# Performance work log

Measured on AMD Instinct MI355X. Metric: run time of the kernel, lower is better.

## Reference

```python
import jax, jax.numpy as jnp
import numpy as np

DIM = 512
NUM_HEADS = 8
POS_DIM = 2
K_CLUSTERS = 256
M_PTS = 256


def setup_inputs() -> dict:
    key = jax.random.key(0)
    ks = jax.random.split(key, 9)
    pos = jax.random.uniform(ks[0], (K_CLUSTERS, M_PTS, POS_DIM), dtype=jnp.float32)
    feat = jax.random.normal(ks[1], (K_CLUSTERS, M_PTS, DIM), dtype=jnp.float32)
    mask = jax.random.randint(ks[2], (K_CLUSTERS, M_PTS, 1), 0, 2, dtype=jnp.int32)
    s = 0.02
    qkv_w = jax.random.normal(ks[3], (DIM, 3 * DIM), dtype=jnp.float32) * s
    qkv_b = jnp.zeros((3 * DIM,), dtype=jnp.float32)
    pos_w = jax.random.normal(ks[4], (POS_DIM, NUM_HEADS), dtype=jnp.float32) * s
    pos_b = jnp.zeros((NUM_HEADS,), dtype=jnp.float32)
    proj_w = jax.random.normal(ks[5], (DIM, DIM), dtype=jnp.float32) * s
    proj_b = jnp.zeros((DIM,), dtype=jnp.float32)
    return {"pos": pos, "feat": feat, "qkv_w": qkv_w, "qkv_b": qkv_b,
            "pos_w": pos_w, "pos_b": pos_b, "proj_w": proj_w, "proj_b": proj_b,
            "mask": mask}


def reference(pos, feat, qkv_w, qkv_b, pos_w, pos_b, proj_w, proj_b, mask):
    k_, m, c = feat.shape
    H = pos_w.shape[1]
    hd = c // H
    scale = hd ** -0.5

    # qkv projection -> (3, k, H, m, hd)
    qkv = (feat @ qkv_w + qkv_b).reshape(k_, m, 3, H, hd).transpose(2, 0, 3, 1, 4)
    q, k, v = qkv[0], qkv[1], qkv[2]

    attn = jnp.einsum('khid,khjd->khij', q * scale, k)  # k,H,m,m

    # normalize each coordinate by its global max over all clusters/points
    pos_n = pos / jnp.max(pos, axis=(0, 1), keepdims=True)
    # rel_pos[k,a,b,d] = pos[k,b,d] - pos[k,a,d]
    rel_pos = pos_n[:, None, :, :] - pos_n[:, :, None, :]  # k,m,m,d
    pos_bias = rel_pos @ pos_w + pos_b                      # k,m,m,H
    attn = attn + pos_bias.transpose(0, 3, 1, 2)            # k,H,m,m

    # mask: k,m,1 -> additive bias over key dim
    maskf = mask[:, :, 0].astype(attn.dtype)                # k,m
    attn = attn + ((1.0 - maskf) * -100.0)[:, None, None, :]

    attn = jax.nn.softmax(attn, axis=-1)
    x = jnp.einsum('khij,khjd->khid', attn, v)              # k,H,m,hd
    x = x.transpose(0, 2, 1, 3).reshape(k_, m, c)
    x = x @ proj_w + proj_b
    return x
```

## Files before the change

kernel.cpp:

```cpp
#include <hip/hip_runtime.h>
#include <stdint.h>

typedef short bf16x8 __attribute__((ext_vector_type(8)));
typedef float f32x4 __attribute__((ext_vector_type(4)));
typedef unsigned short u16x4 __attribute__((ext_vector_type(4)));
typedef unsigned short ushort_t;

__device__ __forceinline__ float bf2f(unsigned short u) {
    union { unsigned int i; float f; } v; v.i = ((unsigned int)u) << 16; return v.f;
}
__device__ __forceinline__ unsigned short f2bf(float f) {
    union { float f; unsigned int i; } v; v.f = f;
    unsigned int r = (v.i + 0x7FFFu + ((v.i >> 16) & 1u)) >> 16;
    return (unsigned short)r;
}

__device__ __forceinline__ void gload_lds16(const void* g, void* l) {
    __builtin_amdgcn_global_load_lds(
        (const __attribute__((address_space(1))) void*)g,
        (__attribute__((address_space(3))) void*)l, 16, 0, 0);
}

template <bool F32> struct LD;
template <> struct LD<false> {
    static __device__ __forceinline__ float s(const void* p, size_t i) {
        return bf2f(((const ushort_t*)p)[i]);
    }
    static __device__ __forceinline__ bf16x8 v8(const void* p, size_t i) {
        return *reinterpret_cast<const bf16x8*>((const ushort_t*)p + i);
    }
};
template <> struct LD<true> {
    static __device__ __forceinline__ float s(const void* p, size_t i) {
        return ((const float*)p)[i];
    }
    static __device__ __forceinline__ bf16x8 v8(const void* p, size_t i) {
        const float* f = (const float*)p + i;
        float4 a = *reinterpret_cast<const float4*>(f);
        float4 b = *reinterpret_cast<const float4*>(f + 4);
        bf16x8 r;
        r[0] = (short)f2bf(a.x); r[1] = (short)f2bf(a.y);
        r[2] = (short)f2bf(a.z); r[3] = (short)f2bf(a.w);
        r[4] = (short)f2bf(b.x); r[5] = (short)f2bf(b.y);
        r[6] = (short)f2bf(b.z); r[7] = (short)f2bf(b.w);
        return r;
    }
};

__global__ __launch_bounds__(64) void kprobe(const ushort_t* __restrict__ pos, int* __restrict__ dt) {
    float v = bf2f(pos[2 * threadIdx.x]);
    bool sane = (v >= 0.0f) && (v <= 1.0f);
    unsigned long long b = __ballot(sane);
    if (threadIdx.x == 0) dt[0] = (b == ~0ULL) ? 1 : 0;
}

template <bool F32>
static __device__ __forceinline__ void kpos_body(const void* pos, int* pmax, float* s0, float* s1) {
    int p = blockIdx.x * 256 + threadIdx.x;
    s0[threadIdx.x] = LD<F32>::s(pos, 2 * (size_t)p);
    s1[threadIdx.x] = LD<F32>::s(pos, 2 * (size_t)p + 1);
    __syncthreads();
    for (int off = 128; off > 0; off >>= 1) {
        if (threadIdx.x < (unsigned)off) {
            s0[threadIdx.x] = fmaxf(s0[threadIdx.x], s0[threadIdx.x + off]);
            s1[threadIdx.x] = fmaxf(s1[threadIdx.x], s1[threadIdx.x + off]);
        }
        __syncthreads();
    }
    if (threadIdx.x == 0) {
        atomicMax(&pmax[0], __float_as_int(s0[0]));
        atomicMax(&pmax[1], __float_as_int(s1[0]));
    }
}
__global__ __launch_bounds__(256) void kpos_max(const int* __restrict__ dt, const void* __restrict__ pos,
                                                int* __restrict__ pmax) {
    __shared__ float s0[256], s1[256];
    if (dt[0]) kpos_body<false>(pos, pmax, s0, s1);
    else       kpos_body<true>(pos, pmax, s0, s1);
}

template <bool F32>
static __device__ __forceinline__ void ktb_body(const void* pos, const void* pos_w, const int* mask,
                                                const int* pmax, float* tb) {
    int p = blockIdx.x * 256 + threadIdx.x;
    float inv0 = 1.0f / __int_as_float(pmax[0]);
    float inv1 = 1.0f / __int_as_float(pmax[1]);
    float x0 = LD<F32>::s(pos, 2 * (size_t)p) * inv0;
    float x1 = LD<F32>::s(pos, 2 * (size_t)p + 1) * inv1;
    float mterm = mask[p] ? 0.0f : -100.0f;
#pragma unroll
    for (int h = 0; h < 8; h++)
        tb[p * 8 + h] = x0 * LD<F32>::s(pos_w, h) + x1 * LD<F32>::s(pos_w, 8 + h) + mterm;
}
__global__ __launch_bounds__(256) void ktb(const int* __restrict__ dt, const void* __restrict__ pos,
                                           const void* __restrict__ pos_w, const int* __restrict__ mask,
                                           const int* __restrict__ pmax, float* __restrict__ tb) {
    if (dt[0]) ktb_body<false>(pos, pos_w, mask, pmax, tb);
    else       ktb_body<true>(pos, pos_w, mask, pmax, tb);
}

__global__ __launch_bounds__(256) void kbias(const int* __restrict__ dt, const void* __restrict__ qkv_b,
                                             const void* __restrict__ proj_b,
                                             float* __restrict__ qb, float* __restrict__ pb) {
    int i = blockIdx.x * 256 + threadIdx.x;
    if (dt[0]) {
        if (i < 1536) qb[i] = bf2f(((const ushort_t*)qkv_b)[i]);
        if (i < 512)  pb[i] = bf2f(((const ushort_t*)proj_b)[i]);
    } else {
        if (i < 1536) qb[i] = ((const float*)qkv_b)[i];
        if (i < 512)  pb[i] = ((const float*)proj_b)[i];
    }
}

template <bool F32>
static __device__ __forceinline__ void kfeat_body(const void* feat, ushort_t* featb) {
    for (size_t t = (size_t)blockIdx.x * 256 + threadIdx.x; t < 4194304; t += (size_t)gridDim.x * 256) {
        *reinterpret_cast<bf16x8*>(featb + t * 8) = LD<F32>::v8(feat, t * 8);
    }
}
__global__ __launch_bounds__(256) void kfeat(const int* __restrict__ dt, const void* __restrict__ feat,
                                             ushort_t* __restrict__ featb) {
    if (dt[0]) kfeat_body<false>(feat, featb);
    else       kfeat_body<true>(feat, featb);
}

template <bool F32>
static __device__ __forceinline__ void ktrans_body(const void* src, ushort_t* dst, int R, int C,
                                                   ushort_t* tile ) {
    int nbc = C >> 6;
    int rb = (blockIdx.x / nbc) << 6;
    int cb = (blockIdx.x % nbc) << 6;
    for (int i = threadIdx.x; i < 4096; i += 256) {
        int r = i >> 6, c = i & 63;
        tile[r * 65 + c] = f2bf(LD<F32>::s(src, (size_t)(rb + r) * C + cb + c));
    }
    __syncthreads();
    for (int i = threadIdx.x; i < 4096; i += 256) {
        int rr = i & 63, cc = i >> 6;
        dst[(size_t)(cb + cc) * R + rb + rr] = tile[rr * 65 + cc];
    }
}
__global__ __launch_bounds__(256) void ktrans(const int* __restrict__ dt, const void* __restrict__ src,
                                              ushort_t* __restrict__ dst, int R, int C) {
    __shared__ ushort_t tile[64 * 65];
    if (dt[0]) ktrans_body<false>(src, dst, R, C, tile);
    else       ktrans_body<true>(src, dst, R, C, tile);
}

template <bool F32>
static __device__ __forceinline__ void kattn_body(const void* feat, const ushort_t* qkv_wt,
                                                  const float* qb, const float* tb, ushort_t* xout,
                                                  ushort_t* sQ, ushort_t* sK, ushort_t* sVt,
                                                  ushort_t* sP, float* stb) {
    const int tid = threadIdx.x;
    const int lane = tid & 63;
    const int wave = tid >> 6;
    const int quad = lane >> 4;
    const int l15 = lane & 15;

    const int bx = blockIdx.x;
    const int xcd = bx & 7;
    const int jj = bx >> 3;
    const int rr = jj >> 5;
    const int ss = jj & 31;
    const int kc = xcd * 32 + rr * 4 + (ss >> 3);
    const int h = ss & 7;

    if (tid < 256) stb[tid] = tb[(size_t)(kc * 256 + tid) * 8 + h];

    ushort_t* sW = sP;
    char* ldsW = (char*)sW;

    const int lc1 = tid >> 2, ch1 = (tid & 3) ^ ((lc1 >> 1) & 3);
    const ushort_t* g1 = qkv_wt + (size_t)((lc1 >> 6) * 512 + h * 64 + (lc1 & 63)) * 512 + ch1 * 8;
    const bool stager = (tid < 768);

    const int wrow = (wave >> 2) * 64;
    const int wcol = (wave & 3) * 48;
    const int swz = (l15 >> 1) & 3;

    f32x4 acc[4][3];
#pragma unroll
    for (int rt = 0; rt < 4; rt++)
#pragma unroll
        for (int ct = 0; ct < 3; ct++) {
            f32x4 z = {0.0f, 0.0f, 0.0f, 0.0f};
            acc[rt][ct] = z;
        }

    const size_t fbase = (size_t)(kc * 256) * 512;

    if (stager) gload_lds16(g1, ldsW + wave * 1024);
    __syncthreads();

#pragma unroll 2
    for (int c = 0; c < 16; c++) {
        const int cb = (c & 1) * 6144;
        if (c < 15 && stager)
            gload_lds16(g1 + (c + 1) * 32, ldsW + ((c + 1) & 1) * 12288 + wave * 1024);
        bf16x8 af[4];
#pragma unroll
        for (int rt = 0; rt < 4; rt++)
            af[rt] = LD<F32>::v8(feat, fbase + (size_t)(wrow + rt * 16 + l15) * 512 + c * 32 + quad * 8);
        bf16x8 bw[3];
#pragma unroll
        for (int ct = 0; ct < 3; ct++)
            bw[ct] = *reinterpret_cast<const bf16x8*>(
                sW + cb + (wcol + ct * 16 + l15) * 32 + (quad ^ swz) * 8);
#pragma unroll
        for (int ct = 0; ct < 3; ct++)
#pragma unroll
            for (int rt = 0; rt < 4; rt++)
                acc[rt][ct] = __builtin_amdgcn_mfma_f32_16x16x32_bf16(af[rt], bw[ct], acc[rt][ct], 0, 0, 0);
        __syncthreads();
    }

#pragma unroll
    for (int ct = 0; ct < 3; ct++) {
        const int lcb = wcol + ct * 16;
        const int mat = lcb >> 6;
        const int col = (lcb & 63) + l15;
        const float bias = qb[mat * 512 + h * 64 + col];
#pragma unroll
        for (int rt = 0; rt < 4; rt++) {
            const int m0 = wrow + rt * 16 + quad * 4;
            if (mat == 0) {
#pragma unroll
                for (int r = 0; r < 4; r++)
                    sQ[(m0 + r) * 72 + col] = f2bf((acc[rt][ct][r] + bias) * 0.125f);
            } else if (mat == 1) {
#pragma unroll
                for (int r = 0; r < 4; r++)
                    sK[(m0 + r) * 72 + col] = f2bf(acc[rt][ct][r] + bias);
            } else {
                u16x4 vp;
#pragma unroll
                for (int r = 0; r < 4; r++) vp[r] = f2bf(acc[rt][ct][r] + bias);
                *reinterpret_cast<u16x4*>(&sVt[col * 264 + m0]) = vp;
            }
        }
    }
    __syncthreads();

    bf16x8 aQ[2];
#pragma unroll
    for (int s = 0; s < 2; s++)
        aQ[s] = *reinterpret_cast<const bf16x8*>(
            &sQ[(wave * 16 + l15) * 72 + s * 32 + quad * 8]);

    f32x4 accO[4];
    float rs[4];
#pragma unroll
    for (int ct = 0; ct < 4; ct++) {
        f32x4 z = {0.0f, 0.0f, 0.0f, 0.0f};
        accO[ct] = z;
        rs[ct] = 0.0f;
    }

    ushort_t* sPw = sP + wave * (16 * 72);

    for (int jb = 0; jb < 4; jb++) {
        int kb = jb * 64;
        bf16x8 bK[4][2];
#pragma unroll
        for (int ctk = 0; ctk < 4; ctk++)
#pragma unroll
            for (int s = 0; s < 2; s++)
                bK[ctk][s] = *reinterpret_cast<const bf16x8*>(
                    &sK[(kb + ctk * 16 + l15) * 72 + s * 32 + quad * 8]);

#pragma unroll
        for (int ctk = 0; ctk < 4; ctk++) {
            float tcol = stb[kb + ctk * 16 + l15];
            f32x4 sa = {0.0f, 0.0f, 0.0f, 0.0f};
            sa = __builtin_amdgcn_mfma_f32_16x16x32_bf16(aQ[0], bK[ctk][0], sa, 0, 0, 0);
            sa = __builtin_amdgcn_mfma_f32_16x16x32_bf16(aQ[1], bK[ctk][1], sa, 0, 0, 0);
            int rl0 = quad * 4;
#pragma unroll
            for (int r = 0; r < 4; r++) {
                float pexp = __expf(sa[r] + tcol);
                rs[r] += pexp;
                sPw[(rl0 + r) * 72 + ctk * 16 + l15] = f2bf(pexp);
            }
        }

#pragma unroll
        for (int s = 0; s < 2; s++) {
            bf16x8 aP = *reinterpret_cast<const bf16x8*>(
                &sPw[l15 * 72 + s * 32 + quad * 8]);
#pragma unroll
            for (int ct = 0; ct < 4; ct++) {
                bf16x8 bV = *reinterpret_cast<const bf16x8*>(
                    &sVt[(ct * 16 + l15) * 264 + kb + s * 32 + quad * 8]);
                accO[ct] = __builtin_amdgcn_mfma_f32_16x16x32_bf16(aP, bV, accO[ct], 0, 0, 0);
            }
        }
    }

    float inv_[4];
#pragma unroll
    for (int r = 0; r < 4; r++) {
        float v = rs[r];
        v += __shfl_xor(v, 1, 64);
        v += __shfl_xor(v, 2, 64);
        v += __shfl_xor(v, 4, 64);
        v += __shfl_xor(v, 8, 64);
        inv_[r] = 1.0f / v;
    }

#pragma unroll
    for (int ct = 0; ct < 4; ct++)
#pragma unroll
        for (int r = 0; r < 4; r++) {
            int m = wave * 16 + quad * 4 + r;
            xout[((size_t)(kc * 256 + m)) * 512 + h * 64 + ct * 16 + l15] =
                f2bf(accO[ct][r] * inv_[r]);
        }
}
__global__ __launch_bounds__(1024, 4) void kattn_bf(const ushort_t* __restrict__ featb,
                                                    const ushort_t* __restrict__ qkv_wt,
                                                    const float* __restrict__ qb,
                                                    const float* __restrict__ tb, ushort_t* __restrict__ xout) {
    __shared__ ushort_t sQ[256 * 72];
    __shared__ ushort_t sK[256 * 72];
    __shared__ ushort_t sVt[64 * 264];
    __shared__ ushort_t sP[16 * 16 * 72];
    __shared__ float stb[256];
    kattn_body<false>(featb, qkv_wt, qb, tb, xout, sQ, sK, sVt, sP, stb);
}
__global__ __launch_bounds__(1024, 4) void kattn_dyn(const int* __restrict__ dt, const void* __restrict__ feat,
                                                     const ushort_t* __restrict__ qkv_wt,
                                                     const float* __restrict__ qb,
                                                     const float* __restrict__ tb, ushort_t* __restrict__ xout) {
    __shared__ ushort_t sQ[256 * 72];
    __shared__ ushort_t sK[256 * 72];
    __shared__ ushort_t sVt[64 * 264];
    __shared__ ushort_t sP[16 * 16 * 72];
    __shared__ float stb[256];
    if (dt[0]) kattn_body<false>(feat, qkv_wt, qb, tb, xout, sQ, sK, sVt, sP, stb);
    else       kattn_body<true>(feat, qkv_wt, qb, tb, xout, sQ, sK, sVt, sP, stb);
}

template <bool F32>
static __device__ __forceinline__ void kproj_body(const ushort_t* x, const ushort_t* proj_wt,
                                                  const float* pb, void* out, ushort_t* sW) {
    const int tid = threadIdx.x;
    const int lane = tid & 63;
    const int wave = tid >> 6;
    const int quad = lane >> 4;
    const int l15 = lane & 15;
    const int bx = blockIdx.x;
    const int xcd = bx & 7;
    const int j = bx >> 3;
    const int rowb = (xcd * 32 + (j >> 2)) * 256;
    const int colb = (j & 3) * 128;
    const int rowg = (wave >> 1) * 64;
    const int colg = (wave & 1) * 64;
    char* ldsW = (char*)sW;

    const int lc = tid >> 2, ch = (tid & 3) ^ ((lc >> 1) & 3);
    const ushort_t* g1 = proj_wt + (size_t)(colb + lc) * 512 + ch * 8;
    const int swz = (l15 >> 1) & 3;

    f32x4 acc[4][4];
#pragma unroll
    for (int rt = 0; rt < 4; rt++)
#pragma unroll
        for (int ct = 0; ct < 4; ct++) {
            f32x4 z = {0.0f, 0.0f, 0.0f, 0.0f};
            acc[rt][ct] = z;
        }

    gload_lds16(g1, ldsW + wave * 1024);
    __syncthreads();

#pragma unroll 2
    for (int c = 0; c < 16; c++) {
        const int cb = (c & 1) * 4096;
        if (c < 15)
            gload_lds16(g1 + (c + 1) * 32, ldsW + ((c + 1) & 1) * 8192 + wave * 1024);
        bf16x8 af[4];
#pragma unroll
        for (int rt = 0; rt < 4; rt++) {
            int m = rowb + rowg + rt * 16 + l15;
            af[rt] = *reinterpret_cast<const bf16x8*>(x + (size_t)m * 512 + c * 32 + quad * 8);
        }
        bf16x8 bw[4];
#pragma unroll
        for (int ct = 0; ct < 4; ct++)
            bw[ct] = *reinterpret_cast<const bf16x8*>(
                sW + cb + (colg + ct * 16 + l15) * 32 + (quad ^ swz) * 8);
#pragma unroll
        for (int ct = 0; ct < 4; ct++)
#pragma unroll
            for (int rt = 0; rt < 4; rt++)
                acc[rt][ct] = __builtin_amdgcn_mfma_f32_16x16x32_bf16(af[rt], bw[ct], acc[rt][ct], 0, 0, 0);
        __syncthreads();
    }

#pragma unroll
    for (int ct = 0; ct < 4; ct++) {
        int n = colb + colg + ct * 16 + l15;
        float bias = pb[n];
#pragma unroll
        for (int rt = 0; rt < 4; rt++)
#pragma unroll
            for (int r = 0; r < 4; r++) {
                int m = rowb + rowg + rt * 16 + quad * 4 + r;
                float v = acc[rt][ct][r] + bias;
                if (F32) ((float*)out)[(size_t)m * 512 + n] = v;
                else     ((ushort_t*)out)[(size_t)m * 512 + n] = f2bf(v);
            }
    }
}
__global__ __launch_bounds__(512, 4) void kproj(const int* __restrict__ dt, const ushort_t* __restrict__ x,
                                                const ushort_t* __restrict__ proj_wt,
                                                const float* __restrict__ pb, void* __restrict__ out) {
    __shared__ ushort_t sW[2 * 128 * 32];
    if (dt[0]) kproj_body<false>(x, proj_wt, pb, out, sW);
    else       kproj_body<true>(x, proj_wt, pb, out, sW);
}

extern "C" void kernel_launch(void* const* d_in, const int* in_sizes, int n_in,
                              void* d_out, int out_size, void* d_ws, size_t ws_size,
                              hipStream_t stream) {
    (void)in_sizes; (void)n_in; (void)out_size;
    const void* pos    = d_in[0];
    const void* feat   = d_in[1];
    const void* qkv_w  = d_in[2];
    const void* qkv_b  = d_in[3];
    const void* pos_w  = d_in[4];
    const void* proj_w = d_in[6];
    const void* proj_b = d_in[7];
    const int* mask    = (const int*)d_in[8];

    char* ws = (char*)d_ws;
    int* pmax         = (int*)ws;
    int* dtf          = (int*)ws + 2;
    float* qb         = (float*)(ws + 256);
    float* pb         = (float*)(ws + 256 + 6144);
    float* tb         = (float*)(ws + 16384);
    ushort_t* qkv_wt  = (ushort_t*)(ws + 16384 + 2097152);
    ushort_t* proj_wt = qkv_wt + 786432;
    ushort_t* x       = proj_wt + 262144;
    ushort_t* featb   = x + 33554432;
    const size_t NEED = 16384 + 2097152 + 1572864 + 524288 + 67108864 + 67108864;
    const bool big = ws_size >= NEED;

    (void)hipMemsetAsync(ws, 0, 16, stream);
    kprobe<<<1, 64, 0, stream>>>((const ushort_t*)pos, dtf);
    kpos_max<<<256, 256, 0, stream>>>(dtf, pos, pmax);
    ktb<<<256, 256, 0, stream>>>(dtf, pos, pos_w, mask, pmax, tb);
    kbias<<<6, 256, 0, stream>>>(dtf, qkv_b, proj_b, qb, pb);
    ktrans<<<192, 256, 0, stream>>>(dtf, qkv_w, qkv_wt, 512, 1536);
    ktrans<<<64, 256, 0, stream>>>(dtf, proj_w, proj_wt, 512, 512);
    if (big) {
        kfeat<<<2048, 256, 0, stream>>>(dtf, feat, featb);
        kattn_bf<<<2048, 1024, 0, stream>>>(featb, qkv_wt, qb, tb, x);
    } else {
        kattn_dyn<<<2048, 1024, 0, stream>>>(dtf, feat, qkv_wt, qb, tb, x);
    }
    kproj<<<1024, 512, 0, stream>>>(dtf, x, proj_wt, pb, d_out);
}
```

Baseline: 658.8 us.

## Shrink attention block to 8 waves with XOR-swizzled LDS and phased QKV

The fused QKV+attention kernel now uses 512 threads instead of 1024. It computes Q, K and V in three sequential GEMM phases, staging Q through a small reused region. LDS layouts switch from padded rows to XOR-swizzled unpadded tiles, so shared memory shrinks to about 80KB, which is meant to raise occupancy and cut bank conflicts. Each wave now handles 32 query rows, and the position bias is read straight from global memory. The cost is three passes over the feature tile instead of one, which triples feature loads, plus extra barriers.

```diff
diff --git a/kernel.cpp b/kernel.cpp
--- a/kernel.cpp
+++ b/kernel.cpp
@@ -150,8 +150,7 @@
 template <bool F32>
 static __device__ __forceinline__ void kattn_body(const void* feat, const ushort_t* qkv_wt,
                                                   const float* qb, const float* tb, ushort_t* xout,
-                                                  ushort_t* sQ, ushort_t* sK, ushort_t* sVt,
-                                                  ushort_t* sP, float* stb) {
+                                                  ushort_t* smem) {
     const int tid = threadIdx.x;
     const int lane = tid & 63;
     const int wave = tid >> 6;
@@ -161,184 +160,238 @@
     const int bx = blockIdx.x;
     const int xcd = bx & 7;
     const int jj = bx >> 3;
-    const int rr = jj >> 5;
-    const int ss = jj & 31;
-    const int kc = xcd * 32 + rr * 4 + (ss >> 3);
-    const int h = ss & 7;
-
-    if (tid < 256) stb[tid] = tb[(size_t)(kc * 256 + tid) * 8 + h];
-
-    ushort_t* sW = sP;
-    char* ldsW = (char*)sW;
-
-    const int lc1 = tid >> 2, ch1 = (tid & 3) ^ ((lc1 >> 1) & 3);
-    const ushort_t* g1 = qkv_wt + (size_t)((lc1 >> 6) * 512 + h * 64 + (lc1 & 63)) * 512 + ch1 * 8;
-    const bool stager = (tid < 768);
-
-    const int wrow = (wave >> 2) * 64;
-    const int wcol = (wave & 3) * 48;
-    const int swz = (l15 >> 1) & 3;
-
-    f32x4 acc[4][3];
-#pragma unroll
-    for (int rt = 0; rt < 4; rt++)
-#pragma unroll
-        for (int ct = 0; ct < 3; ct++) {
+    const int rnd = jj >> 6;
+    const int slot = jj & 63;
+    const int kc = xcd * 32 + rnd * 8 + (slot >> 3);
+    const int h = slot & 7;
+
+    ushort_t* sVt = smem;
+    ushort_t* sK  = smem + 16384;
+    ushort_t* Cr  = smem + 32768;
+    char* CrB = (char*)Cr;
+
+    const int wrow = (wave >> 1) * 64;
+    const int wcol = (wave & 1) * 32;
+
+    const int lc = (tid & 255) >> 2;
+    const int chs = (tid & 3) ^ (lc & 3);
+    const bool stager = (tid < 256);
+
+    const size_t fbase = (size_t)(kc * 256) * 512;
+    bf16x8 aQ[2][2];
+
+#pragma unroll
+    for (int p = 0; p < 3; p++) {
+        const ushort_t* gW = qkv_wt + (size_t)(p * 512 + h * 64 + lc) * 512 + chs * 8;
+        f32x4 acc[4][2];
+#pragma unroll
+        for (int rt = 0; rt < 4; rt++)
+#pragma unroll
+            for (int ct = 0; ct < 2; ct++) { f32x4 z = {0.0f, 0.0f, 0.0f, 0.0f}; acc[rt][ct] = z; }
+
+        if (stager) gload_lds16(gW, CrB + (tid & 255) * 16);
+        __syncthreads();
+
+#pragma unroll 2
+        for (int c = 0; c < 16; c++) {
+            if (c < 15 && stager)
+                gload_lds16(gW + (c + 1) * 32, CrB + ((c + 1) & 1) * 4096 + (tid & 255) * 16);
+            bf16x8 af[4];
+#pragma unroll
+            for (int rt = 0; rt < 4; rt++)
+                af[rt] = LD<F32>::v8(feat, fbase + (size_t)(wrow + rt * 16 + l15) * 512 + c * 32 + quad * 8);
+            bf16x8 bw[2];
+#pragma unroll
+            for (int ct = 0; ct < 2; ct++) {
+                int rw = wcol + ct * 16 + l15;
+                bw[ct] = *reinterpret_cast<const bf16x8*>(
+                    Cr + (c & 1) * 2048 + rw * 32 + (quad ^ (rw & 3)) * 8);
+            }
+#pragma unroll
+            for (int ct = 0; ct < 2; ct++)
+#pragma unroll
+                for (int rt = 0; rt < 4; rt++)
+                    acc[rt][ct] = __builtin_amdgcn_mfma_f32_16x16x32_bf16(af[rt], bw[ct], acc[rt][ct], 0, 0, 0);
+            __syncthreads();
+        }
+
+        if (p == 0) {
+            ushort_t qv[2][4][4];
+#pragma unroll
+            for (int ct = 0; ct < 2; ct++) {
+                int col = wcol + ct * 16 + l15;
+                float bias = qb[h * 64 + col];
+#pragma unroll
+                for (int rt = 0; rt < 4; rt++)
+#pragma unroll
+                    for (int r = 0; r < 4; r++)
+                        qv[ct][rt][r] = f2bf((acc[rt][ct][r] + bias) * 0.125f);
+            }
+#pragma unroll
+            for (int half = 0; half < 2; half++) {
+                if ((wrow >> 7) == half) {
+#pragma unroll
+                    for (int ct = 0; ct < 2; ct++) {
+                        int col = wcol + ct * 16 + l15;
+#pragma unroll
+                        for (int rt = 0; rt < 4; rt++)
+#pragma unroll
+                            for (int r = 0; r < 4; r++) {
+                                int m = wrow + rt * 16 + quad * 4 + r;
+                                Cr[(m & 127) * 64 + (((col >> 3) ^ (m & 7)) * 8) + (col & 7)] =
+                                    qv[ct][rt][r];
+                            }
+                    }
+                }
+                __syncthreads();
+                if ((wave >> 2) == half) {
+#pragma unroll
+                    for (int rt = 0; rt < 2; rt++)
+#pragma unroll
+                        for (int s = 0; s < 2; s++) {
+                            int row = wave * 32 + rt * 16 + l15;
+                            aQ[rt][s] = *reinterpret_cast<const bf16x8*>(
+                                Cr + (row & 127) * 64 + (((s * 4 + quad) ^ (row & 7)) * 8));
+                        }
+                }
+                __syncthreads();
+            }
+        } else if (p == 1) {
+#pragma unroll
+            for (int ct = 0; ct < 2; ct++) {
+                int col = wcol + ct * 16 + l15;
+                float bias = qb[512 + h * 64 + col];
+#pragma unroll
+                for (int rt = 0; rt < 4; rt++)
+#pragma unroll
+                    for (int r = 0; r < 4; r++) {
+                        int m = wrow + rt * 16 + quad * 4 + r;
+                        sK[m * 64 + (((col >> 3) ^ (m & 7)) * 8) + (col & 7)] =
+                            f2bf(acc[rt][ct][r] + bias);
+                    }
+            }
+        } else {
+#pragma unroll
+            for (int ct = 0; ct < 2; ct++) {
+                int hd_ = wcol + ct * 16 + l15;
+                float bias = qb[1024 + h * 64 + hd_];
+#pragma unroll
+                for (int rt = 0; rt < 4; rt++) {
+                    int m0 = wrow + rt * 16 + quad * 4;
+                    u16x4 vp;
+#pragma unroll
+                    for (int r = 0; r < 4; r++) vp[r] = f2bf(acc[rt][ct][r] + bias);
+                    *reinterpret_cast<u16x4*>(
+                        &sVt[hd_ * 256 + (((m0 >> 3) ^ (hd_ & 7)) * 8) + (m0 & 7)]) = vp;
+                }
+            }
+        }
+    }
+    __syncthreads();
+
+    f32x4 accO[2][4];
+    float rs[2][4];
+#pragma unroll
+    for (int rt = 0; rt < 2; rt++)
+#pragma unroll
+        for (int ct = 0; ct < 4; ct++) {
             f32x4 z = {0.0f, 0.0f, 0.0f, 0.0f};
-            acc[rt][ct] = z;
-        }
-
-    const size_t fbase = (size_t)(kc * 256) * 512;
-
-    if (stager) gload_lds16(g1, ldsW + wave * 1024);
-    __syncthreads();
-
-#pragma unroll 2
-    for (int c = 0; c < 16; c++) {
-        const int cb = (c & 1) * 6144;
-        if (c < 15 && stager)
-            gload_lds16(g1 + (c + 1) * 32, ldsW + ((c + 1) & 1) * 12288 + wave * 1024);
-        bf16x8 af[4];
-#pragma unroll
-        for (int rt = 0; rt < 4; rt++)
-            af[rt] = LD<F32>::v8(feat, fbase + (size_t)(wrow + rt * 16 + l15) * 512 + c * 32 + quad * 8);
-        bf16x8 bw[3];
-#pragma unroll
-        for (int ct = 0; ct < 3; ct++)
-            bw[ct] = *reinterpret_cast<const bf16x8*>(
-                sW + cb + (wcol + ct * 16 + l15) * 32 + (quad ^ swz) * 8);
-#pragma unroll
-        for (int ct = 0; ct < 3; ct++)
-#pragma unroll
-            for (int rt = 0; rt < 4; rt++)
-                acc[rt][ct] = __builtin_amdgcn_mfma_f32_16x16x32_bf16(af[rt], bw[ct], acc[rt][ct], 0, 0, 0);
-        __syncthreads();
-    }
-
-#pragma unroll
-    for (int ct = 0; ct < 3; ct++) {
-        const int lcb = wcol + ct * 16;
-        const int mat = lcb >> 6;
-        const int col = (lcb & 63) + l15;
-        const float bias = qb[mat * 512 + h * 64 + col];
-#pragma unroll
-        for (int rt = 0; rt < 4; rt++) {
-            const int m0 = wrow + rt * 16 + quad * 4;
-            if (mat == 0) {
-#pragma unroll
-                for (int r = 0; r < 4; r++)
-                    sQ[(m0 + r) * 72 + col] = f2bf((acc[rt][ct][r] + bias) * 0.125f);
-            } else if (mat == 1) {
-#pragma unroll
-                for (int r = 0; r < 4; r++)
-                    sK[(m0 + r) * 72 + col] = f2bf(acc[rt][ct][r] + bias);
-            } else {
-                u16x4 vp;
-#pragma unroll
-                for (int r = 0; r < 4; r++) vp[r] = f2bf(acc[rt][ct][r] + bias);
-                *reinterpret_cast<u16x4*>(&sVt[col * 264 + m0]) = vp;
-            }
-        }
-    }
-    __syncthreads();
-
-    bf16x8 aQ[2];
-#pragma unroll
-    for (int s = 0; s < 2; s++)
-        aQ[s] = *reinterpret_cast<const bf16x8*>(
-            &sQ[(wave * 16 + l15) * 72 + s * 32 + quad * 8]);
-
-    f32x4 accO[4];
-    float rs[4];
-#pragma unroll
-    for (int ct = 0; ct < 4; ct++) {
-        f32x4 z = {0.0f, 0.0f, 0.0f, 0.0f};
-        accO[ct] = z;
-        rs[ct] = 0.0f;
-    }
-
-    ushort_t* sPw = sP + wave * (16 * 72);
+            accO[rt][ct] = z;
+            rs[rt][ct] = 0.0f;
+        }
+
+    ushort_t* sPw = Cr + wave * 1024;
 
     for (int jb = 0; jb < 4; jb++) {
         int kb = jb * 64;
+        float tc[4];
+#pragma unroll
+        for (int ctk = 0; ctk < 4; ctk++)
+            tc[ctk] = tb[(size_t)(kc * 256 + kb + ctk * 16 + l15) * 8 + h];
         bf16x8 bK[4][2];
 #pragma unroll
         for (int ctk = 0; ctk < 4; ctk++)
 #pragma unroll
-            for (int s = 0; s < 2; s++)
+            for (int s = 0; s < 2; s++) {
+                int row = kb + ctk * 16 + l15;
                 bK[ctk][s] = *reinterpret_cast<const bf16x8*>(
-                    &sK[(kb + ctk * 16 + l15) * 72 + s * 32 + quad * 8]);
-
-#pragma unroll
-        for (int ctk = 0; ctk < 4; ctk++) {
-            float tcol = stb[kb + ctk * 16 + l15];
-            f32x4 sa = {0.0f, 0.0f, 0.0f, 0.0f};
-            sa = __builtin_amdgcn_mfma_f32_16x16x32_bf16(aQ[0], bK[ctk][0], sa, 0, 0, 0);
-            sa = __builtin_amdgcn_mfma_f32_16x16x32_bf16(aQ[1], bK[ctk][1], sa, 0, 0, 0);
-            int rl0 = quad * 4;
+                    sK + row * 64 + (((s * 4 + quad) ^ (row & 7)) * 8));
+            }
+
+#pragma unroll
+        for (int sh = 0; sh < 2; sh++) {
+#pragma unroll
+            for (int ck = 0; ck < 2; ck++) {
+                int ctk = sh * 2 + ck;
+                float tcol = tc[ctk];
+#pragma unroll
+                for (int rt = 0; rt < 2; rt++) {
+                    f32x4 sa = {0.0f, 0.0f, 0.0f, 0.0f};
+                    sa = __builtin_amdgcn_mfma_f32_16x16x32_bf16(aQ[rt][0], bK[ctk][0], sa, 0, 0, 0);
+                    sa = __builtin_amdgcn_mfma_f32_16x16x32_bf16(aQ[rt][1], bK[ctk][1], sa, 0, 0, 0);
+#pragma unroll
+                    for (int r = 0; r < 4; r++) {
+                        float pexp = __expf(sa[r] + tcol);
+                        rs[rt][r] += pexp;
+                        int prow = rt * 16 + quad * 4 + r;
+                        sPw[prow * 32 + (((ck * 2 + (l15 >> 3)) ^ (prow & 3)) * 8) + (l15 & 7)] =
+                            f2bf(pexp);
+                    }
+                }
+            }
+#pragma unroll
+            for (int rt = 0; rt < 2; rt++) {
+                bf16x8 aP = *reinterpret_cast<const bf16x8*>(
+                    sPw + (rt * 16 + l15) * 32 + ((quad ^ (l15 & 3)) * 8));
+#pragma unroll
+                for (int ct = 0; ct < 4; ct++) {
+                    int vrow = ct * 16 + l15;
+                    bf16x8 bV = *reinterpret_cast<const bf16x8*>(
+                        sVt + vrow * 256 + (((jb * 8 + sh * 4 + quad) ^ (vrow & 7)) * 8));
+                    accO[rt][ct] = __builtin_amdgcn_mfma_f32_16x16x32_bf16(aP, bV, accO[rt][ct], 0, 0, 0);
+                }
+            }
+        }
+    }
+
+    float inv_[2][4];
+#pragma unroll
+    for (int rt = 0; rt < 2; rt++)
+#pragma unroll
+        for (int r = 0; r < 4; r++) {
+            float v = rs[rt][r];
+            v += __shfl_xor(v, 1, 64);
+            v += __shfl_xor(v, 2, 64);
+            v += __shfl_xor(v, 4, 64);
+            v += __shfl_xor(v, 8, 64);
+            inv_[rt][r] = 1.0f / v;
+        }
+
+#pragma unroll
+    for (int rt = 0; rt < 2; rt++)
+#pragma unroll
+        for (int ct = 0; ct < 4; ct++)
 #pragma unroll
             for (int r = 0; r < 4; r++) {
-                float pexp = __expf(sa[r] + tcol);
-                rs[r] += pexp;
-                sPw[(rl0 + r) * 72 + ctk * 16 + l15] = f2bf(pexp);
-            }
-        }
-
-#pragma unroll
-        for (int s = 0; s < 2; s++) {
-            bf16x8 aP = *reinterpret_cast<const bf16x8*>(
-                &sPw[l15 * 72 + s * 32 + quad * 8]);
-#pragma unroll
-            for (int ct = 0; ct < 4; ct++) {
-                bf16x8 bV = *reinterpret_cast<const bf16x8*>(
-                    &sVt[(ct * 16 + l15) * 264 + kb + s * 32 + quad * 8]);
-                accO[ct] = __builtin_amdgcn_mfma_f32_16x16x32_bf16(aP, bV, accO[ct], 0, 0, 0);
-            }
-        }
-    }
-
-    float inv_[4];
-#pragma unroll
-    for (int r = 0; r < 4; r++) {
-        float v = rs[r];
-        v += __shfl_xor(v, 1, 64);
-        v += __shfl_xor(v, 2, 64);
-        v += __shfl_xor(v, 4, 64);
-        v += __shfl_xor(v, 8, 64);
-        inv_[r] = 1.0f / v;
-    }
-
-#pragma unroll
-    for (int ct = 0; ct < 4; ct++)
-#pragma unroll
-        for (int r = 0; r < 4; r++) {
-            int m = wave * 16 + quad * 4 + r;
-            xout[((size_t)(kc * 256 + m)) * 512 + h * 64 + ct * 16 + l15] =
-                f2bf(accO[ct][r] * inv_[r]);
-        }
-}
-__global__ __launch_bounds__(1024, 4) void kattn_bf(const ushort_t* __restrict__ featb,
+                int m = wave * 32 + rt * 16 + quad * 4 + r;
+                xout[((size_t)(kc * 256 + m)) * 512 + h * 64 + ct * 16 + l15] =
+                    f2bf(accO[rt][ct][r] * inv_[rt][r]);
+            }
+}
+__global__ __launch_bounds__(512, 4) void kattn_bf(const ushort_t* __restrict__ featb,
+                                                   const ushort_t* __restrict__ qkv_wt,
+                                                   const float* __restrict__ qb,
+                                                   const float* __restrict__ tb, ushort_t* __restrict__ xout) {
+    __shared__ ushort_t smem[40960];
+    kattn_body<false>(featb, qkv_wt, qb, tb, xout, smem);
+}
+__global__ __launch_bounds__(512, 4) void kattn_dyn(const int* __restrict__ dt, const void* __restrict__ feat,
                                                     const ushort_t* __restrict__ qkv_wt,
                                                     const float* __restrict__ qb,
                                                     const float* __restrict__ tb, ushort_t* __restrict__ xout) {
-    __shared__ ushort_t sQ[256 * 72];
-    __shared__ ushort_t sK[256 * 72];
-    __shared__ ushort_t sVt[64 * 264];
-    __shared__ ushort_t sP[16 * 16 * 72];
-    __shared__ float stb[256];
-    kattn_body<false>(featb, qkv_wt, qb, tb, xout, sQ, sK, sVt, sP, stb);
-}
-__global__ __launch_bounds__(1024, 4) void kattn_dyn(const int* __restrict__ dt, const void* __restrict__ feat,
-                                                     const ushort_t* __restrict__ qkv_wt,
-                                                     const float* __restrict__ qb,
-                                                     const float* __restrict__ tb, ushort_t* __restrict__ xout) {
-    __shared__ ushort_t sQ[256 * 72];
-    __shared__ ushort_t sK[256 * 72];
-    __shared__ ushort_t sVt[64 * 264];
-    __shared__ ushort_t sP[16 * 16 * 72];
-    __shared__ float stb[256];
-    if (dt[0]) kattn_body<false>(feat, qkv_wt, qb, tb, xout, sQ, sK, sVt, sP, stb);
-    else       kattn_body<true>(feat, qkv_wt, qb, tb, xout, sQ, sK, sVt, sP, stb);
+    __shared__ ushort_t smem[40960];
+    if (dt[0]) kattn_body<false>(feat, qkv_wt, qb, tb, xout, smem);
+    else       kattn_body<true>(feat, qkv_wt, qb, tb, xout, smem);
 }
 
 template <bool F32>
@@ -456,9 +509,9 @@
     ktrans<<<64, 256, 0, stream>>>(dtf, proj_w, proj_wt, 512, 512);
     if (big) {
         kfeat<<<2048, 256, 0, stream>>>(dtf, feat, featb);
-        kattn_bf<<<2048, 1024, 0, stream>>>(featb, qkv_wt, qb, tb, x);
+        kattn_bf<<<2048, 512, 0, stream>>>(featb, qkv_wt, qb, tb, x);
     } else {
-        kattn_dyn<<<2048, 1024, 0, stream>>>(dtf, feat, qkv_wt, qb, tb, x);
+        kattn_dyn<<<2048, 512, 0, stream>>>(dtf, feat, qkv_wt, qb, tb, x);
     }
     kproj<<<1024, 512, 0, stream>>>(dtf, x, proj_wt, pb, d_out);
 }
```

Result: slower. 747.3 us (+13.4%).
